# Optimization experiments

Hardware: AMD Instinct MI355X
Metric: run time of the kernel (lower is better)

The kernel has to match this reference:

```python
import jax, jax.numpy as jnp
import numpy as np

B_SCALE = 1.3195079565048218
N_LEVELS = 16
BASE_RES = 16
MAX_PARAMS = 2 ** 19
N_POINTS = 1048576
PRIMES = (1, 2654435761, 805459861)  # uint32 hash primes (Instant-NGP)


def _level_meta():
    offsets, sizes, inds = [], [], []
    off = 0
    for i in range(N_LEVELS):
        res = int(np.ceil(BASE_RES * np.exp(i * np.log(B_SCALE)) - 1.0)) + 1
        p = res ** 3
        if p % 8 != 0:
            p = ((p + 7) // 8) * 8
        p = min(MAX_PARAMS, p)
        offsets.append(off)
        sizes.append(p)
        inds.append(res ** 3 <= p)  # dense (under_hash) vs hashed level
        off += p
    return offsets, sizes, inds, off


OFFSETS, SIZES, INDICATORS, TOTAL_PARAMS = _level_meta()
TOTAL_HASH_SIZE = TOTAL_PARAMS * 2  # == 11445040


def _encode_level(x01, table2, level):
    # x01: [N,3] in [0,1]; table2: [total_params, 2]
    scale = np.float32(BASE_RES * np.exp(level * np.log(B_SCALE)) - 1.0)
    resolution = np.uint32(np.ceil(scale) + 1)
    map_size = np.uint32(SIZES[level])
    pos = x01 * scale + 0.5
    grid_f = jnp.floor(pos)
    frac = pos - grid_f                           # [N,3] trilinear weights
    grid = grid_f.astype(jnp.uint32)              # [N,3]
    feat = jnp.zeros((x01.shape[0], 2), dtype=table2.dtype)
    primes = np.array(PRIMES, dtype=np.uint32)
    stride = np.array([1, int(resolution), int(resolution) * int(resolution)], dtype=np.uint32)
    for idx in range(8):  # 8 grid corners
        sel = np.array([(idx >> d) & 1 for d in range(3)], dtype=np.uint32)
        corner = grid + sel                       # [N,3] uint32
        w = jnp.prod(jnp.where(sel[None, :] == 1, frac, 1.0 - frac), axis=-1)  # [N]
        if INDICATORS[level]:
            c = corner * stride[None, :]
            h = c[:, 0] + c[:, 1] + c[:, 2]       # under_hash (dense indexing)
        else:
            c = corner * primes[None, :]          # uint32 wraparound multiply
            h = c[:, 0] ^ c[:, 1] ^ c[:, 2]       # fast_hash
        index = (h % map_size).astype(jnp.int32) + np.int32(OFFSETS[level])
        feat = feat + w[:, None] * table2[index]  # gather + trilinear blend
    return feat


def setup_inputs() -> dict:
    key = jax.random.key(0)
    k1, k2 = jax.random.split(key)
    positions = jax.random.uniform(k1, (N_POINTS, 3), dtype=jnp.float32, minval=-1.0, maxval=1.0)
    # random_initialize: (rand*2-1)*1e-4
    hash_table = jax.random.uniform(k2, (TOTAL_HASH_SIZE,), dtype=jnp.float32, minval=-1e-4, maxval=1e-4)
    return {"positions": positions, "hash_table": hash_table}


def reference(positions, hash_table):
    x01 = (positions + 1.0) * 0.5  # bound = 1
    table2 = hash_table.reshape(-1, 2)
    feats = [_encode_level(x01, table2, l) for l in range(N_LEVELS)]
    return jnp.concatenate(feats, axis=-1)  # [N, 32]
```

## Files before the change

### kernel.cpp

```cpp
#include <hip/hip_runtime.h>
#include <math.h>
#include <stdint.h>

#define NLV 16
#define NDENSE 6
#define NHASH 10
#define SORT_RES 32
#define NBINS (SORT_RES * SORT_RES * SORT_RES)

typedef float evf2 __attribute__((ext_vector_type(2)));

struct Params {
  float scale[NLV];
  uint32_t res[NLV];
  uint32_t msize[NLV];
  uint32_t offset[NLV];
};

struct ParamsD {
  float scale[NDENSE];
  uint32_t res[NDENSE];
  uint32_t msize[NDENSE];
  uint32_t offset[NDENSE];
};

__device__ __forceinline__ float ntload(const float* p) {
  return __builtin_nontemporal_load(p);
}

__device__ __forceinline__ uint32_t cell_key(float xr, float yr, float zr) {
  float x01 = (xr + 1.0f) * 0.5f;
  float y01 = (yr + 1.0f) * 0.5f;
  float z01 = (zr + 1.0f) * 0.5f;
  int cx = (int)(x01 * (float)SORT_RES);
  int cy = (int)(y01 * (float)SORT_RES);
  int cz = (int)(z01 * (float)SORT_RES);
  cx = cx < 0 ? 0 : (cx > SORT_RES-1 ? SORT_RES-1 : cx);
  cy = cy < 0 ? 0 : (cy > SORT_RES-1 ? SORT_RES-1 : cy);
  cz = cz < 0 ? 0 : (cz > SORT_RES-1 ? SORT_RES-1 : cz);
  return (uint32_t)(cx | (cy << 5) | (cz << 10));
}

__global__ __launch_bounds__(256) void zero_bins_kernel(uint32_t* bins) {
  int i = blockIdx.x * 256 + threadIdx.x;
  if (i < NBINS) bins[i] = 0u;
}

__global__ __launch_bounds__(256) void hist_kernel(
    const float* __restrict__ positions, uint32_t* __restrict__ bins, int n) {
  int p = blockIdx.x * 256 + threadIdx.x;
  if (p >= n) return;
  float x = positions[3*p], y = positions[3*p+1], z = positions[3*p+2];
  atomicAdd(&bins[cell_key(x, y, z)], 1u);
}

__global__ __launch_bounds__(1024) void scan_kernel(
    const uint32_t* __restrict__ bins, uint32_t* __restrict__ cursor) {
  __shared__ uint32_t lds[1024];
  int t = threadIdx.x;
  uint32_t local[32];
  uint32_t s = 0;
  #pragma unroll
  for (int j = 0; j < 32; ++j) { local[j] = bins[t*32 + j]; s += local[j]; }
  lds[t] = s;
  __syncthreads();
  for (int off = 1; off < 1024; off <<= 1) {
    uint32_t v = (t >= off) ? lds[t - off] : 0u;
    __syncthreads();
    lds[t] += v;
    __syncthreads();
  }
  uint32_t run = lds[t] - s;
  #pragma unroll
  for (int j = 0; j < 32; ++j) { cursor[t*32 + j] = run; run += local[j]; }
}

__global__ __launch_bounds__(256) void scatter_kernel(
    const float* __restrict__ positions, uint32_t* __restrict__ cursor,
    float* __restrict__ sortedPos, uint32_t* __restrict__ origIdx, int n) {
  int p = blockIdx.x * 256 + threadIdx.x;
  if (p >= n) return;
  float x = positions[3*p], y = positions[3*p+1], z = positions[3*p+2];
  uint32_t k = cell_key(x, y, z);
  uint32_t dst = atomicAdd(&cursor[k], 1u);
  sortedPos[3*dst]   = x;
  sortedPos[3*dst+1] = y;
  sortedPos[3*dst+2] = z;
  origIdx[dst] = p;
}

__global__ __launch_bounds__(256) void hash_level_kernel(
    const float* __restrict__ positions,
    const float* __restrict__ tbl,
    float2* __restrict__ tmp,
    float scale, uint32_t mask, int n)
{
  int t = blockIdx.x * 256 + threadIdx.x;
  int p0 = t * 2;
  if (p0 >= n) return;

  float xx[2], yy[2], zz[2];
  {
    evf2 a = __builtin_nontemporal_load(reinterpret_cast<const evf2*>(positions + 3*p0));
    evf2 b = __builtin_nontemporal_load(reinterpret_cast<const evf2*>(positions + 3*p0 + 2));
    evf2 c = __builtin_nontemporal_load(reinterpret_cast<const evf2*>(positions + 3*p0 + 4));
    xx[0] = a.x; yy[0] = a.y; zz[0] = b.x;
    xx[1] = b.y; yy[1] = c.x; zz[1] = c.y;
  }

  float r0[2], r1[2];
  #pragma unroll
  for (int q = 0; q < 2; ++q) {
    float x = (xx[q] + 1.0f) * 0.5f;
    float y = (yy[q] + 1.0f) * 0.5f;
    float z = (zz[q] + 1.0f) * 0.5f;

    float px = x * scale + 0.5f;
    float py = y * scale + 0.5f;
    float pz = z * scale + 0.5f;
    float fx = floorf(px), fy = floorf(py), fz = floorf(pz);
    float tx = px - fx, ty = py - fy, tz = pz - fz;
    uint32_t gx = (uint32_t)fx, gy = (uint32_t)fy, gz = (uint32_t)fz;

    float wxa = 1.0f - tx, wxb = tx;
    float wy_[2] = {1.0f - ty, ty};
    float wz_[2] = {1.0f - tz, tz};

    float f0 = 0.0f, f1 = 0.0f;

    if ((gx & 1u) == 0u) {
      #pragma unroll
      for (int cyz = 0; cyz < 4; ++cyz) {
        uint32_t cy = gy + (cyz & 1u);
        uint32_t cz = gz + (cyz >> 1);
        uint32_t hy = (cy * 2654435761u) ^ (cz * 805459861u);
        uint32_t ha = (gx ^ hy) & mask;
        float wyz = wy_[cyz & 1u] * wz_[cyz >> 1];
        float wa = wxa * wyz, wb = wxb * wyz;
        const float4 t4 = *reinterpret_cast<const float4*>(tbl + 2u * (ha & ~1u));
        float2 ta, tb;
        if (ha & 1u) { ta.x = t4.z; ta.y = t4.w; tb.x = t4.x; tb.y = t4.y; }
        else         { ta.x = t4.x; ta.y = t4.y; tb.x = t4.z; tb.y = t4.w; }
        f0 += wa * ta.x; f1 += wa * ta.y;
        f0 += wb * tb.x; f1 += wb * tb.y;
      }
    } else {
      #pragma unroll
      for (int cyz = 0; cyz < 4; ++cyz) {
        uint32_t cy = gy + (cyz & 1u);
        uint32_t cz = gz + (cyz >> 1);
        uint32_t hy = (cy * 2654435761u) ^ (cz * 805459861u);
        uint32_t ha = (gx ^ hy) & mask;
        uint32_t hb = ((gx + 1u) ^ hy) & mask;
        float wyz = wy_[cyz & 1u] * wz_[cyz >> 1];
        float wa = wxa * wyz, wb = wxb * wyz;
        const float2 ta = *reinterpret_cast<const float2*>(tbl + 2u * ha);
        const float2 tb = *reinterpret_cast<const float2*>(tbl + 2u * hb);
        f0 += wa * ta.x; f1 += wa * ta.y;
        f0 += wb * tb.x; f1 += wb * tb.y;
      }
    }
    r0[q] = f0; r1[q] = f1;
  }

  evf2 v0; v0.x = r0[0]; v0.y = r1[0];
  __builtin_nontemporal_store(v0, reinterpret_cast<evf2*>(tmp + p0));
  if (p0 + 1 < n) {
    evf2 v1; v1.x = r0[1]; v1.y = r1[1];
    __builtin_nontemporal_store(v1, reinterpret_cast<evf2*>(tmp + p0 + 1));
  }
}

__global__ __launch_bounds__(256) void dense_kernel(
    const float* __restrict__ positions,
    const float* __restrict__ table,
    float2* __restrict__ tmp,
    ParamsD prm, int n)
{
  int p = blockIdx.x * 256 + threadIdx.x;
  if (p >= n) return;

  float x = (ntload(positions + 3*p+0) + 1.0f) * 0.5f;
  float y = (ntload(positions + 3*p+1) + 1.0f) * 0.5f;
  float z = (ntload(positions + 3*p+2) + 1.0f) * 0.5f;

  #pragma unroll
  for (int l = 0; l < NDENSE; ++l) {
    const float s = prm.scale[l];
    const uint32_t res = prm.res[l];
    const uint32_t ms = prm.msize[l];
    const float* __restrict__ tbl = table + 2u * prm.offset[l];
    const uint32_t res2 = res * res;

    float px = x * s + 0.5f;
    float py = y * s + 0.5f;
    float pz = z * s + 0.5f;
    float fx = floorf(px), fy = floorf(py), fz = floorf(pz);
    float tx = px - fx, ty = py - fy, tz = pz - fz;
    uint32_t gx = (uint32_t)fx, gy = (uint32_t)fy, gz = (uint32_t)fz;

    float wxa = 1.0f - tx, wxb = tx;
    float wy_[2] = {1.0f - ty, ty};
    float wz_[2] = {1.0f - tz, tz};

    float f0 = 0.0f, f1 = 0.0f;
    #pragma unroll
    for (int cyz = 0; cyz < 4; ++cyz) {
      uint32_t cy = gy + (cyz & 1u);
      uint32_t cz = gz + ((cyz >> 1) & 1u);
      uint32_t h = gx + cy * res + cz * res2;
      if (h >= ms) h -= ms;
      float wyz = wy_[cyz & 1u] * wz_[(cyz >> 1) & 1u];
      float2 ta, tb;
      if (h + 1u < ms) {
        const float4 t4 = *reinterpret_cast<const float4*>(tbl + 2u * h);
        ta.x = t4.x; ta.y = t4.y; tb.x = t4.z; tb.y = t4.w;
      } else {
        ta = *reinterpret_cast<const float2*>(tbl + 2u * h);
        tb = *reinterpret_cast<const float2*>(tbl);
      }
      float wa = wxa * wyz, wb = wxb * wyz;
      f0 += wa * ta.x; f1 += wa * ta.y;
      f0 += wb * tb.x; f1 += wb * tb.y;
    }
    evf2 v; v.x = f0; v.y = f1;
    __builtin_nontemporal_store(v,
        reinterpret_cast<evf2*>(tmp + (size_t)(NHASH + l) * n + p));
  }
}

__global__ __launch_bounds__(256) void pack_scatter_kernel(
    const float2* __restrict__ tmp,
    const uint32_t* __restrict__ origIdx,
    float* __restrict__ out, int n)
{
  __shared__ float lds[256 * 33];
  int t = threadIdx.x;
  int base = blockIdx.x * 256;
  int p = base + t;

  if (p < n) {
    #pragma unroll
    for (int j = 0; j < NDENSE; ++j) {
      evf2 v = __builtin_nontemporal_load(
          reinterpret_cast<const evf2*>(tmp + (size_t)(NHASH + j) * n + p));
      lds[t*33 + 2*j]     = v.x;
      lds[t*33 + 2*j + 1] = v.y;
    }
    #pragma unroll
    for (int j = 0; j < NHASH; ++j) {
      evf2 v = __builtin_nontemporal_load(
          reinterpret_cast<const evf2*>(tmp + (size_t)j * n + p));
      lds[t*33 + 12 + 2*j]     = v.x;
      lds[t*33 + 12 + 2*j + 1] = v.y;
    }
  }
  __syncthreads();

  if (base + 256 <= n) {
    int qr = t >> 3, r = t & 7;
    #pragma unroll
    for (int k = 0; k < 8; ++k) {
      int q = k * 32 + qr;
      uint32_t oi = origIdx[base + q];
      float4 v = make_float4(lds[q*33 + r*4], lds[q*33 + r*4 + 1],
                             lds[q*33 + r*4 + 2], lds[q*33 + r*4 + 3]);
      reinterpret_cast<float4*>(out + (size_t)oi * 32u)[r] = v;
    }
  } else if (p < n) {
    uint32_t oi = origIdx[p];
    float4* o = reinterpret_cast<float4*>(out + (size_t)oi * 32u);
    #pragma unroll
    for (int k = 0; k < 8; ++k)
      o[k] = make_float4(lds[t*33 + 4*k], lds[t*33 + 4*k + 1],
                         lds[t*33 + 4*k + 2], lds[t*33 + 4*k + 3]);
  }
}

__global__ __launch_bounds__(256) void stream_pack_kernel(
    const float2* __restrict__ tmp, float* __restrict__ out, int n)
{
  int p = blockIdx.x * 256 + threadIdx.x;
  if (p >= n) return;

  evf2 dv[NDENSE];
  #pragma unroll
  for (int j = 0; j < NDENSE; ++j)
    dv[j] = __builtin_nontemporal_load(
        reinterpret_cast<const evf2*>(tmp + (size_t)(NHASH + j) * n + p));
  evf2 hv[NHASH];
  #pragma unroll
  for (int j = 0; j < NHASH; ++j)
    hv[j] = __builtin_nontemporal_load(
        reinterpret_cast<const evf2*>(tmp + (size_t)j * n + p));

  float4* o = reinterpret_cast<float4*>(out + (size_t)p * 32u);
  #pragma unroll
  for (int j = 0; j < 3; ++j)
    o[j] = make_float4(dv[2*j].x, dv[2*j].y, dv[2*j+1].x, dv[2*j+1].y);
  #pragma unroll
  for (int j = 0; j < 5; ++j)
    o[3 + j] = make_float4(hv[2*j].x, hv[2*j].y, hv[2*j+1].x, hv[2*j+1].y);
}

__global__ __launch_bounds__(256) void hash_enc_kernel(
    const float* __restrict__ positions,
    const float* __restrict__ table,
    float* __restrict__ out,
    Params prm, int n)
{
  int p = blockIdx.x * 256 + threadIdx.x;
  if (p >= n) return;

  float x = (positions[3*p+0] + 1.0f) * 0.5f;
  float y = (positions[3*p+1] + 1.0f) * 0.5f;
  float z = (positions[3*p+2] + 1.0f) * 0.5f;

  float acc[32];

  #pragma unroll
  for (int l = 0; l < NLV; ++l) {
    const float s = prm.scale[l];
    const uint32_t res = prm.res[l];
    const uint32_t ms = prm.msize[l];
    const uint32_t off = prm.offset[l];

    float px = x * s + 0.5f;
    float py = y * s + 0.5f;
    float pz = z * s + 0.5f;
    float fx = floorf(px), fy = floorf(py), fz = floorf(pz);
    float tx = px - fx, ty = py - fy, tz = pz - fz;
    uint32_t gx = (uint32_t)fx, gy = (uint32_t)fy, gz = (uint32_t)fz;

    float wx[2] = {1.0f - tx, tx};
    float wy[2] = {1.0f - ty, ty};
    float wz[2] = {1.0f - tz, tz};

    float f0 = 0.0f, f1 = 0.0f;
    #pragma unroll
    for (int c = 0; c < 8; ++c) {
      uint32_t cx = gx + (c & 1u);
      uint32_t cy = gy + ((c >> 1) & 1u);
      uint32_t cz = gz + ((c >> 2) & 1u);
      uint32_t h;
      if (l < NDENSE) {
        h = cx + cy * res + cz * res * res;
        if (h >= ms) h -= ms;
      } else {
        h = cx ^ (cy * 2654435761u) ^ (cz * 805459861u);
        h &= (ms - 1u);
      }
      float w = (wx[c & 1u] * wy[(c >> 1) & 1u]) * wz[(c >> 2) & 1u];
      const float2 t = *reinterpret_cast<const float2*>(table + 2u * (h + off));
      f0 += w * t.x;
      f1 += w * t.y;
    }
    acc[2*l]   = f0;
    acc[2*l+1] = f1;
  }

  float4* o = reinterpret_cast<float4*>(out + (size_t)p * 32u);
  #pragma unroll
  for (int k = 0; k < 8; ++k)
    o[k] = make_float4(acc[4*k+0], acc[4*k+1], acc[4*k+2], acc[4*k+3]);
}

extern "C" void kernel_launch(void* const* d_in, const int* in_sizes, int n_in,
                              void* d_out, int out_size, void* d_ws, size_t ws_size,
                              hipStream_t stream) {
  const float* positions = (const float*)d_in[0];
  const float* table     = (const float*)d_in[1];
  float* out             = (float*)d_out;
  int n = in_sizes[0] / 3;

  Params prm;
  const double lnb = log(1.3195079565048218);
  uint32_t off = 0;
  for (int l = 0; l < NLV; ++l) {
    double sd = 16.0 * exp((double)l * lnb) - 1.0;
    uint32_t res_meta = (uint32_t)ceil(sd) + 1u;
    uint64_t p3 = (uint64_t)res_meta * res_meta * res_meta;
    uint64_t ps = (p3 % 8ull) ? ((p3 + 7ull) / 8ull) * 8ull : p3;
    if (ps > (1ull << 19)) ps = 1ull << 19;
    float sf = (float)sd;
    uint32_t res_enc = (uint32_t)(ceilf(sf) + 1.0f);
    prm.scale[l]  = sf;
    prm.res[l]    = res_enc;
    prm.msize[l]  = (uint32_t)ps;
    prm.offset[l] = off;
    off += (uint32_t)ps;
  }
  ParamsD pd;
  for (int l = 0; l < NDENSE; ++l) {
    pd.scale[l] = prm.scale[l]; pd.res[l] = prm.res[l];
    pd.msize[l] = prm.msize[l]; pd.offset[l] = prm.offset[l];
  }

  dim3 block(256);
  dim3 gfull((n + 255) / 256);
  dim3 ghash((n/2 + 255) / 256);

  size_t tmp_b  = (size_t)NLV * n * sizeof(float2);
  size_t sp_off = tmp_b;
  size_t oi_off = sp_off + (size_t)3 * n * sizeof(float);
  size_t bn_off = oi_off + (size_t)n * sizeof(uint32_t);
  size_t cu_off = bn_off + (size_t)NBINS * sizeof(uint32_t);
  size_t total  = cu_off + (size_t)NBINS * sizeof(uint32_t);
  size_t ws16   = tmp_b;

  char* wsb = (char*)d_ws;

  if (ws_size >= total && (n % 2) == 0) {
    float2*   tmp       = (float2*)wsb;
    float*    sortedPos = (float*)(wsb + sp_off);
    uint32_t* origIdx   = (uint32_t*)(wsb + oi_off);
    uint32_t* bins      = (uint32_t*)(wsb + bn_off);
    uint32_t* cursor    = (uint32_t*)(wsb + cu_off);

    hipLaunchKernelGGL(zero_bins_kernel, dim3((NBINS + 255) / 256), block, 0, stream, bins);
    hipLaunchKernelGGL(hist_kernel, gfull, block, 0, stream, positions, bins, n);
    hipLaunchKernelGGL(scan_kernel, dim3(1), dim3(1024), 0, stream, bins, cursor);
    hipLaunchKernelGGL(scatter_kernel, gfull, block, 0, stream,
                       positions, cursor, sortedPos, origIdx, n);

    for (int l = NDENSE; l < NLV; ++l) {
      hipLaunchKernelGGL(hash_level_kernel, ghash, block, 0, stream,
                         sortedPos, table + 2u * prm.offset[l],
                         tmp + (size_t)(l - NDENSE) * n,
                         prm.scale[l], prm.msize[l] - 1u, n);
    }
    hipLaunchKernelGGL(dense_kernel, gfull, block, 0, stream,
                       sortedPos, table, tmp, pd, n);
    hipLaunchKernelGGL(pack_scatter_kernel, gfull, block, 0, stream,
                       tmp, origIdx, out, n);
  } else if (ws_size >= ws16 && (n % 2) == 0) {
    float2* tmp = (float2*)d_ws;
    for (int l = NDENSE; l < NLV; ++l) {
      hipLaunchKernelGGL(hash_level_kernel, ghash, block, 0, stream,
                         positions, table + 2u * prm.offset[l],
                         tmp + (size_t)(l - NDENSE) * n,
                         prm.scale[l], prm.msize[l] - 1u, n);
    }
    hipLaunchKernelGGL(dense_kernel, gfull, block, 0, stream,
                       positions, table, tmp, pd, n);
    hipLaunchKernelGGL(stream_pack_kernel, gfull, block, 0, stream,
                       tmp, out, n);
  } else {
    hipLaunchKernelGGL(hash_enc_kernel, gfull, block, 0, stream,
                       positions, table, out, prm, n);
  }
}
```

Measured before the change: 448.7 us.

## Fuse dense levels into pack-scatter and interleave sorted positions with indices

Merges the dense-level encoding into the final pack/scatter kernel, so the six dense-level outputs never go through the temporary workspace. Sorted positions and original indices are packed into a single 16-byte record, which the hash-level kernels and the fused kernel read with one vector load each. The histogram and scatter kernels now handle four points per thread using float4 loads. In exchange, the fused kernel carries more register and LDS pressure, and the sorted path now requires n divisible by 4.

```diff
diff --git a/kernel.cpp b/kernel.cpp
--- a/kernel.cpp
+++ b/kernel.cpp
@@ -9,6 +9,7 @@
 #define NBINS (SORT_RES * SORT_RES * SORT_RES)
 
 typedef float evf2 __attribute__((ext_vector_type(2)));
+typedef unsigned int evu4 __attribute__((ext_vector_type(4)));
 
 struct Params {
   float scale[NLV];
@@ -48,10 +49,16 @@
 
 __global__ __launch_bounds__(256) void hist_kernel(
     const float* __restrict__ positions, uint32_t* __restrict__ bins, int n) {
-  int p = blockIdx.x * 256 + threadIdx.x;
-  if (p >= n) return;
-  float x = positions[3*p], y = positions[3*p+1], z = positions[3*p+2];
-  atomicAdd(&bins[cell_key(x, y, z)], 1u);
+  int t = blockIdx.x * 256 + threadIdx.x;
+  int p0 = t * 4;
+  if (p0 >= n) return;
+  const float4 A = *reinterpret_cast<const float4*>(positions + 3*p0);
+  const float4 B = *reinterpret_cast<const float4*>(positions + 3*p0 + 4);
+  const float4 C = *reinterpret_cast<const float4*>(positions + 3*p0 + 8);
+  atomicAdd(&bins[cell_key(A.x, A.y, A.z)], 1u);
+  atomicAdd(&bins[cell_key(A.w, B.x, B.y)], 1u);
+  atomicAdd(&bins[cell_key(B.z, B.w, C.x)], 1u);
+  atomicAdd(&bins[cell_key(C.y, C.z, C.w)], 1u);
 }
 
 __global__ __launch_bounds__(1024) void scan_kernel(
@@ -77,20 +84,31 @@
 
 __global__ __launch_bounds__(256) void scatter_kernel(
     const float* __restrict__ positions, uint32_t* __restrict__ cursor,
-    float* __restrict__ sortedPos, uint32_t* __restrict__ origIdx, int n) {
-  int p = blockIdx.x * 256 + threadIdx.x;
-  if (p >= n) return;
-  float x = positions[3*p], y = positions[3*p+1], z = positions[3*p+2];
-  uint32_t k = cell_key(x, y, z);
-  uint32_t dst = atomicAdd(&cursor[k], 1u);
-  sortedPos[3*dst]   = x;
-  sortedPos[3*dst+1] = y;
-  sortedPos[3*dst+2] = z;
-  origIdx[dst] = p;
+    evu4* __restrict__ spi, int n) {
+  int t = blockIdx.x * 256 + threadIdx.x;
+  int p0 = t * 4;
+  if (p0 >= n) return;
+  const float4 A = *reinterpret_cast<const float4*>(positions + 3*p0);
+  const float4 B = *reinterpret_cast<const float4*>(positions + 3*p0 + 4);
+  const float4 C = *reinterpret_cast<const float4*>(positions + 3*p0 + 8);
+  float xs[4] = {A.x, A.w, B.z, C.y};
+  float ys[4] = {A.y, B.x, B.w, C.z};
+  float zs[4] = {A.z, B.y, C.x, C.w};
+  #pragma unroll
+  for (int q = 0; q < 4; ++q) {
+    uint32_t k = cell_key(xs[q], ys[q], zs[q]);
+    uint32_t dst = atomicAdd(&cursor[k], 1u);
+    evu4 v;
+    v.x = __float_as_uint(xs[q]);
+    v.y = __float_as_uint(ys[q]);
+    v.z = __float_as_uint(zs[q]);
+    v.w = (uint32_t)(p0 + q);
+    spi[dst] = v;
+  }
 }
 
 __global__ __launch_bounds__(256) void hash_level_kernel(
-    const float* __restrict__ positions,
+    const evu4* __restrict__ spi,
     const float* __restrict__ tbl,
     float2* __restrict__ tmp,
     float scale, uint32_t mask, int n)
@@ -99,14 +117,11 @@
   int p0 = t * 2;
   if (p0 >= n) return;
 
-  float xx[2], yy[2], zz[2];
-  {
-    evf2 a = __builtin_nontemporal_load(reinterpret_cast<const evf2*>(positions + 3*p0));
-    evf2 b = __builtin_nontemporal_load(reinterpret_cast<const evf2*>(positions + 3*p0 + 2));
-    evf2 c = __builtin_nontemporal_load(reinterpret_cast<const evf2*>(positions + 3*p0 + 4));
-    xx[0] = a.x; yy[0] = a.y; zz[0] = b.x;
-    xx[1] = b.y; yy[1] = c.x; zz[1] = c.y;
-  }
+  evu4 a = __builtin_nontemporal_load(spi + p0);
+  evu4 b = (p0 + 1 < n) ? __builtin_nontemporal_load(spi + p0 + 1) : a;
+  float xx[2] = {__uint_as_float(a.x), __uint_as_float(b.x)};
+  float yy[2] = {__uint_as_float(a.y), __uint_as_float(b.y)};
+  float zz[2] = {__uint_as_float(a.z), __uint_as_float(b.z)};
 
   float r0[2], r1[2];
   #pragma unroll
@@ -171,7 +186,159 @@
   }
 }
 
-__global__ __launch_bounds__(256) void dense_kernel(
+__global__ __launch_bounds__(256) void dense_pack2_kernel(
+    const evu4* __restrict__ spi,
+    const float* __restrict__ table,
+    const float2* __restrict__ tmp,
+    float* __restrict__ out,
+    ParamsD prm, int n)
+{
+  __shared__ float lds[256 * 33];
+  __shared__ uint32_t lds_oi[256];
+  int t = threadIdx.x;
+  int base = blockIdx.x * 256;
+  int p = base + t;
+
+  if (p < n) {
+    evu4 a = __builtin_nontemporal_load(spi + p);
+    float x = (__uint_as_float(a.x) + 1.0f) * 0.5f;
+    float y = (__uint_as_float(a.y) + 1.0f) * 0.5f;
+    float z = (__uint_as_float(a.z) + 1.0f) * 0.5f;
+    lds_oi[t] = a.w;
+
+    #pragma unroll
+    for (int l = 0; l < NDENSE; ++l) {
+      const float s = prm.scale[l];
+      const uint32_t res = prm.res[l];
+      const uint32_t ms = prm.msize[l];
+      const float* __restrict__ tbl = table + 2u * prm.offset[l];
+      const uint32_t res2 = res * res;
+
+      float px = x * s + 0.5f;
+      float py = y * s + 0.5f;
+      float pz = z * s + 0.5f;
+      float fx = floorf(px), fy = floorf(py), fz = floorf(pz);
+      float tx = px - fx, ty = py - fy, tz = pz - fz;
+      uint32_t gx = (uint32_t)fx, gy = (uint32_t)fy, gz = (uint32_t)fz;
+
+      float wxa = 1.0f - tx, wxb = tx;
+      float wy_[2] = {1.0f - ty, ty};
+      float wz_[2] = {1.0f - tz, tz};
+
+      float f0 = 0.0f, f1 = 0.0f;
+      #pragma unroll
+      for (int cyz = 0; cyz < 4; ++cyz) {
+        uint32_t cy = gy + (cyz & 1u);
+        uint32_t cz = gz + ((cyz >> 1) & 1u);
+        uint32_t h = gx + cy * res + cz * res2;
+        if (h >= ms) h -= ms;
+        float wyz = wy_[cyz & 1u] * wz_[(cyz >> 1) & 1u];
+        float2 ta, tb;
+        if (h + 1u < ms) {
+          const float4 t4 = *reinterpret_cast<const float4*>(tbl + 2u * h);
+          ta.x = t4.x; ta.y = t4.y; tb.x = t4.z; tb.y = t4.w;
+        } else {
+          ta = *reinterpret_cast<const float2*>(tbl + 2u * h);
+          tb = *reinterpret_cast<const float2*>(tbl);
+        }
+        float wa = wxa * wyz, wb = wxb * wyz;
+        f0 += wa * ta.x; f1 += wa * ta.y;
+        f0 += wb * tb.x; f1 += wb * tb.y;
+      }
+      lds[t*33 + 2*l]     = f0;
+      lds[t*33 + 2*l + 1] = f1;
+    }
+
+    #pragma unroll
+    for (int j = 0; j < NHASH; ++j) {
+      evf2 v = __builtin_nontemporal_load(
+          reinterpret_cast<const evf2*>(tmp + (size_t)j * n + p));
+      lds[t*33 + 12 + 2*j]     = v.x;
+      lds[t*33 + 12 + 2*j + 1] = v.y;
+    }
+  }
+  __syncthreads();
+
+  if (base + 256 <= n) {
+    int qr = t >> 3, r = t & 7;
+    #pragma unroll
+    for (int k = 0; k < 8; ++k) {
+      int q = k * 32 + qr;
+      uint32_t oi = lds_oi[q];
+      float4 v = make_float4(lds[q*33 + r*4], lds[q*33 + r*4 + 1],
+                             lds[q*33 + r*4 + 2], lds[q*33 + r*4 + 3]);
+      reinterpret_cast<float4*>(out + (size_t)oi * 32u)[r] = v;
+    }
+  } else if (p < n) {
+    uint32_t oi = lds_oi[t];
+    float4* o = reinterpret_cast<float4*>(out + (size_t)oi * 32u);
+    #pragma unroll
+    for (int k = 0; k < 8; ++k)
+      o[k] = make_float4(lds[t*33 + 4*k], lds[t*33 + 4*k + 1],
+                         lds[t*33 + 4*k + 2], lds[t*33 + 4*k + 3]);
+  }
+}
+
+__global__ __launch_bounds__(256) void hash_level_unsorted_kernel(
+    const float* __restrict__ positions,
+    const float* __restrict__ tbl,
+    float2* __restrict__ tmp,
+    float scale, uint32_t mask, int n)
+{
+  int t = blockIdx.x * 256 + threadIdx.x;
+  int p0 = t * 2;
+  if (p0 >= n) return;
+
+  float xx[2], yy[2], zz[2];
+  {
+    evf2 a = __builtin_nontemporal_load(reinterpret_cast<const evf2*>(positions + 3*p0));
+    evf2 b = __builtin_nontemporal_load(reinterpret_cast<const evf2*>(positions + 3*p0 + 2));
+    evf2 c = __builtin_nontemporal_load(reinterpret_cast<const evf2*>(positions + 3*p0 + 4));
+    xx[0] = a.x; yy[0] = a.y; zz[0] = b.x;
+    xx[1] = b.y; yy[1] = c.x; zz[1] = c.y;
+  }
+
+  float r0[2], r1[2];
+  #pragma unroll
+  for (int q = 0; q < 2; ++q) {
+    float x = (xx[q] + 1.0f) * 0.5f;
+    float y = (yy[q] + 1.0f) * 0.5f;
+    float z = (zz[q] + 1.0f) * 0.5f;
+    float px = x * scale + 0.5f;
+    float py = y * scale + 0.5f;
+    float pz = z * scale + 0.5f;
+    float fx = floorf(px), fy = floorf(py), fz = floorf(pz);
+    float tx = px - fx, ty = py - fy, tz = pz - fz;
+    uint32_t gx = (uint32_t)fx, gy = (uint32_t)fy, gz = (uint32_t)fz;
+    float wxa = 1.0f - tx, wxb = tx;
+    float wy_[2] = {1.0f - ty, ty};
+    float wz_[2] = {1.0f - tz, tz};
+    float f0 = 0.0f, f1 = 0.0f;
+    #pragma unroll
+    for (int cyz = 0; cyz < 4; ++cyz) {
+      uint32_t cy = gy + (cyz & 1u);
+      uint32_t cz = gz + (cyz >> 1);
+      uint32_t hy = (cy * 2654435761u) ^ (cz * 805459861u);
+      uint32_t ha = (gx ^ hy) & mask;
+      uint32_t hb = ((gx + 1u) ^ hy) & mask;
+      float wyz = wy_[cyz & 1u] * wz_[cyz >> 1];
+      float wa = wxa * wyz, wb = wxb * wyz;
+      const float2 ta = *reinterpret_cast<const float2*>(tbl + 2u * ha);
+      const float2 tb = *reinterpret_cast<const float2*>(tbl + 2u * hb);
+      f0 += wa * ta.x; f1 += wa * ta.y;
+      f0 += wb * tb.x; f1 += wb * tb.y;
+    }
+    r0[q] = f0; r1[q] = f1;
+  }
+  evf2 v0; v0.x = r0[0]; v0.y = r1[0];
+  __builtin_nontemporal_store(v0, reinterpret_cast<evf2*>(tmp + p0));
+  if (p0 + 1 < n) {
+    evf2 v1; v1.x = r0[1]; v1.y = r1[1];
+    __builtin_nontemporal_store(v1, reinterpret_cast<evf2*>(tmp + p0 + 1));
+  }
+}
+
+__global__ __launch_bounds__(256) void dense_unsorted_kernel(
     const float* __restrict__ positions,
     const float* __restrict__ table,
     float2* __restrict__ tmp,
@@ -191,18 +358,15 @@
     const uint32_t ms = prm.msize[l];
     const float* __restrict__ tbl = table + 2u * prm.offset[l];
     const uint32_t res2 = res * res;
-
     float px = x * s + 0.5f;
     float py = y * s + 0.5f;
     float pz = z * s + 0.5f;
     float fx = floorf(px), fy = floorf(py), fz = floorf(pz);
     float tx = px - fx, ty = py - fy, tz = pz - fz;
     uint32_t gx = (uint32_t)fx, gy = (uint32_t)fy, gz = (uint32_t)fz;
-
     float wxa = 1.0f - tx, wxb = tx;
     float wy_[2] = {1.0f - ty, ty};
     float wz_[2] = {1.0f - tz, tz};
-
     float f0 = 0.0f, f1 = 0.0f;
     #pragma unroll
     for (int cyz = 0; cyz < 4; ++cyz) {
@@ -229,60 +393,11 @@
   }
 }
 
-__global__ __launch_bounds__(256) void pack_scatter_kernel(
-    const float2* __restrict__ tmp,
-    const uint32_t* __restrict__ origIdx,
-    float* __restrict__ out, int n)
-{
-  __shared__ float lds[256 * 33];
-  int t = threadIdx.x;
-  int base = blockIdx.x * 256;
-  int p = base + t;
-
-  if (p < n) {
-    #pragma unroll
-    for (int j = 0; j < NDENSE; ++j) {
-      evf2 v = __builtin_nontemporal_load(
-          reinterpret_cast<const evf2*>(tmp + (size_t)(NHASH + j) * n + p));
-      lds[t*33 + 2*j]     = v.x;
-      lds[t*33 + 2*j + 1] = v.y;
-    }
-    #pragma unroll
-    for (int j = 0; j < NHASH; ++j) {
-      evf2 v = __builtin_nontemporal_load(
-          reinterpret_cast<const evf2*>(tmp + (size_t)j * n + p));
-      lds[t*33 + 12 + 2*j]     = v.x;
-      lds[t*33 + 12 + 2*j + 1] = v.y;
-    }
-  }
-  __syncthreads();
-
-  if (base + 256 <= n) {
-    int qr = t >> 3, r = t & 7;
-    #pragma unroll
-    for (int k = 0; k < 8; ++k) {
-      int q = k * 32 + qr;
-      uint32_t oi = origIdx[base + q];
-      float4 v = make_float4(lds[q*33 + r*4], lds[q*33 + r*4 + 1],
-                             lds[q*33 + r*4 + 2], lds[q*33 + r*4 + 3]);
-      reinterpret_cast<float4*>(out + (size_t)oi * 32u)[r] = v;
-    }
-  } else if (p < n) {
-    uint32_t oi = origIdx[p];
-    float4* o = reinterpret_cast<float4*>(out + (size_t)oi * 32u);
-    #pragma unroll
-    for (int k = 0; k < 8; ++k)
-      o[k] = make_float4(lds[t*33 + 4*k], lds[t*33 + 4*k + 1],
-                         lds[t*33 + 4*k + 2], lds[t*33 + 4*k + 3]);
-  }
-}
-
 __global__ __launch_bounds__(256) void stream_pack_kernel(
     const float2* __restrict__ tmp, float* __restrict__ out, int n)
 {
   int p = blockIdx.x * 256 + threadIdx.x;
   if (p >= n) return;
-
   evf2 dv[NDENSE];
   #pragma unroll
   for (int j = 0; j < NDENSE; ++j)
@@ -293,7 +408,6 @@
   for (int j = 0; j < NHASH; ++j)
     hv[j] = __builtin_nontemporal_load(
         reinterpret_cast<const evf2*>(tmp + (size_t)j * n + p));
-
   float4* o = reinterpret_cast<float4*>(out + (size_t)p * 32u);
   #pragma unroll
   for (int j = 0; j < 3; ++j)
@@ -324,18 +438,15 @@
     const uint32_t res = prm.res[l];
     const uint32_t ms = prm.msize[l];
     const uint32_t off = prm.offset[l];
-
     float px = x * s + 0.5f;
     float py = y * s + 0.5f;
     float pz = z * s + 0.5f;
     float fx = floorf(px), fy = floorf(py), fz = floorf(pz);
     float tx = px - fx, ty = py - fy, tz = pz - fz;
     uint32_t gx = (uint32_t)fx, gy = (uint32_t)fy, gz = (uint32_t)fz;
-
     float wx[2] = {1.0f - tx, tx};
     float wy[2] = {1.0f - ty, ty};
     float wz[2] = {1.0f - tz, tz};
-
     float f0 = 0.0f, f1 = 0.0f;
     #pragma unroll
     for (int c = 0; c < 8; ++c) {
@@ -399,49 +510,46 @@
   dim3 block(256);
   dim3 gfull((n + 255) / 256);
   dim3 ghash((n/2 + 255) / 256);
-
-  size_t tmp_b  = (size_t)NLV * n * sizeof(float2);
+  dim3 gquad((n/4 + 255) / 256);
+
+  size_t tmp_b  = (size_t)NHASH * n * sizeof(float2);
   size_t sp_off = tmp_b;
-  size_t oi_off = sp_off + (size_t)3 * n * sizeof(float);
-  size_t bn_off = oi_off + (size_t)n * sizeof(uint32_t);
+  size_t bn_off = sp_off + (size_t)n * sizeof(evu4);
   size_t cu_off = bn_off + (size_t)NBINS * sizeof(uint32_t);
   size_t total  = cu_off + (size_t)NBINS * sizeof(uint32_t);
-  size_t ws16   = tmp_b;
+  size_t ws16   = (size_t)NLV * n * sizeof(float2);
 
   char* wsb = (char*)d_ws;
 
-  if (ws_size >= total && (n % 2) == 0) {
-    float2*   tmp       = (float2*)wsb;
-    float*    sortedPos = (float*)(wsb + sp_off);
-    uint32_t* origIdx   = (uint32_t*)(wsb + oi_off);
-    uint32_t* bins      = (uint32_t*)(wsb + bn_off);
-    uint32_t* cursor    = (uint32_t*)(wsb + cu_off);
+  if (ws_size >= total && (n % 4) == 0) {
+    float2*   tmp    = (float2*)wsb;
+    evu4*     spi    = (evu4*)(wsb + sp_off);
+    uint32_t* bins   = (uint32_t*)(wsb + bn_off);
+    uint32_t* cursor = (uint32_t*)(wsb + cu_off);
 
     hipLaunchKernelGGL(zero_bins_kernel, dim3((NBINS + 255) / 256), block, 0, stream, bins);
-    hipLaunchKernelGGL(hist_kernel, gfull, block, 0, stream, positions, bins, n);
+    hipLaunchKernelGGL(hist_kernel, gquad, block, 0, stream, positions, bins, n);
     hipLaunchKernelGGL(scan_kernel, dim3(1), dim3(1024), 0, stream, bins, cursor);
-    hipLaunchKernelGGL(scatter_kernel, gfull, block, 0, stream,
-                       positions, cursor, sortedPos, origIdx, n);
+    hipLaunchKernelGGL(scatter_kernel, gquad, block, 0, stream,
+                       positions, cursor, spi, n);
 
     for (int l = NDENSE; l < NLV; ++l) {
       hipLaunchKernelGGL(hash_level_kernel, ghash, block, 0, stream,
-                         sortedPos, table + 2u * prm.offset[l],
+                         spi, table + 2u * prm.offset[l],
                          tmp + (size_t)(l - NDENSE) * n,
                          prm.scale[l], prm.msize[l] - 1u, n);
     }
-    hipLaunchKernelGGL(dense_kernel, gfull, block, 0, stream,
-                       sortedPos, table, tmp, pd, n);
-    hipLaunchKernelGGL(pack_scatter_kernel, gfull, block, 0, stream,
-                       tmp, origIdx, out, n);
+    hipLaunchKernelGGL(dense_pack2_kernel, gfull, block, 0, stream,
+                       spi, table, tmp, out, pd, n);
   } else if (ws_size >= ws16 && (n % 2) == 0) {
     float2* tmp = (float2*)d_ws;
     for (int l = NDENSE; l < NLV; ++l) {
-      hipLaunchKernelGGL(hash_level_kernel, ghash, block, 0, stream,
+      hipLaunchKernelGGL(hash_level_unsorted_kernel, ghash, block, 0, stream,
                          positions, table + 2u * prm.offset[l],
                          tmp + (size_t)(l - NDENSE) * n,
                          prm.scale[l], prm.msize[l] - 1u, n);
     }
-    hipLaunchKernelGGL(dense_kernel, gfull, block, 0, stream,
+    hipLaunchKernelGGL(dense_unsorted_kernel, gfull, block, 0, stream,
                        positions, table, tmp, pd, n);
     hipLaunchKernelGGL(stream_pack_kernel, gfull, block, 0, stream,
                        tmp, out, n);
```

After: 436.2 us. 1.03x faster.
